# Performance work log

Measured on AMD Instinct MI355X. Metric: run time of the kernel, lower is better.

Reference implementation:

```python
import jax, jax.numpy as jnp
import numpy as np

B, T, V, E, U = 4096, 80, 10000, 100, 512


def setup_inputs() -> dict:
    key = jax.random.key(0)
    ks = jax.random.split(key, 8)
    s = 0.05  # small init scale to keep tanh unsaturated
    return {
        "tokens": jax.random.randint(ks[0], (B, T), 0, V),
        "emb": jax.random.normal(ks[1], (V, E), jnp.float32),
        "W0": jax.random.normal(ks[2], (E, U), jnp.float32) * s,
        "U0": jax.random.normal(ks[3], (U, U), jnp.float32) * s,
        "b0": jnp.zeros((U,), jnp.float32),
        "W1": jax.random.normal(ks[4], (U, U), jnp.float32) * s,
        "U1": jax.random.normal(ks[5], (U, U), jnp.float32) * s,
        "b1": jnp.zeros((U,), jnp.float32),
        "Wout": jax.random.normal(ks[6], (U, 1), jnp.float32) * s,
        "bout": jnp.zeros((1,), jnp.float32),
    }


def reference(tokens, emb, W0, U0, b0, W1, U1, b1, Wout, bout):
    # Embedding lookup: [B, T, E]
    x = emb[tokens]
    batch = tokens.shape[0]
    units = W0.shape[1]
    h0 = jnp.zeros((batch, units), x.dtype)
    h1 = jnp.zeros((batch, units), x.dtype)

    def step(carry, xt):
        h0, h1 = carry
        # SimpleRNNCell (inference: dropout inactive): h' = tanh(x@W + h@U + b)
        h0 = jnp.tanh(xt @ W0 + h0 @ U0 + b0)
        h1 = jnp.tanh(h0 @ W1 + h1 @ U1 + b1)
        return (h0, h1), None

    (h0, h1), _ = jax.lax.scan(step, (h0, h1), jnp.swapaxes(x, 0, 1))  # time-major scan
    return jax.nn.sigmoid(h1 @ Wout + bout)  # [B, 1]
```

## Files before the change

### kernel.cpp

```cpp
#include <hip/hip_runtime.h>
#include <hip/hip_bf16.h>
#include <math.h>

#define Tt 80
#define Vv 10000
#define Ee 100
#define Uu 512
#define ROWS 16
#define NBLK 256
#define SLICE_B 32768
#define NSLICE 24

typedef __attribute__((ext_vector_type(4))) int i32x4;
typedef __attribute__((ext_vector_type(4))) unsigned u32x4;

__device__ __forceinline__ i32x4 as_i4(u32x4 v) {
    union { u32x4 u; i32x4 i; } p;
    p.u = v;
    return p.i;
}

__device__ __forceinline__ float tanh_fast(float x) {
    float z = fminf(fmaxf(x, -15.f), 15.f);
    float e = __expf(2.f * z);
    return (e - 1.f) / (e + 1.f);
}

__global__ __launch_bounds__(512) void k_embw0(const float* __restrict__ emb,
                                               const float* __restrict__ W0,
                                               const float* __restrict__ b0,
                                               float* __restrict__ embW0) {
    __shared__ float semb[4][Ee];
    int v0 = blockIdx.x * 4;
    int tid = threadIdx.x;
    if (tid < 4 * Ee) semb[tid / Ee][tid % Ee] = emb[(v0 + tid / Ee) * Ee + tid % Ee];
    __syncthreads();
    float b = b0[tid];
    for (int vl = 0; vl < 4; ++vl) {
        float a = 0.f;
        #pragma unroll 4
        for (int e = 0; e < Ee; ++e) a += semb[vl][e] * W0[e * Uu + tid];
        embW0[(v0 + vl) * Uu + tid] = a + b;
    }
}

__global__ __launch_bounds__(256) void k_scale(const float* __restrict__ U0,
                                               const float* __restrict__ W1,
                                               const float* __restrict__ U1,
                                               float* __restrict__ scl) {
    int w = blockIdx.x * 4 + (threadIdx.x >> 6);
    int lane = threadIdx.x & 63;
    int mat = w >> 9, col = w & 511;
    const float* src = (mat == 0) ? U0 : (mat == 1) ? W1 : U1;
    float v = 0.f;
    #pragma unroll
    for (int i = 0; i < 8; ++i) v = fmaxf(v, fabsf(src[(lane + i * 64) * Uu + col]));
    #pragma unroll
    for (int o = 32; o; o >>= 1) v = fmaxf(v, __shfl_xor(v, o));
    if (lane == 0) scl[w] = v;
}

__global__ __launch_bounds__(256) void k_pack(const float* __restrict__ U0,
                                              const float* __restrict__ W1,
                                              const float* __restrict__ U1,
                                              const float* __restrict__ scl,
                                              char* __restrict__ pW) {
    int gid = blockIdx.x * 256 + threadIdx.x;
    int S = gid >> 11;
    int ntg = (gid >> 6) & 31;
    int lane = gid & 63;
    int col = ntg * 16 + (lane & 15);
    const float* src;
    int slot;
    float a;
    if (S < 8) { src = U0; slot = S; a = scl[col]; }
    else {
        int s2 = S - 8;
        slot = s2 >> 1;
        src = (s2 & 1) ? U1 : W1;
        a = fmaxf(scl[512 + col], scl[1024 + col]);
    }
    float inv = 127.0f / a;
    int k0 = slot * 64 + (lane >> 4) * 16;
    union { char c[16]; uint4 u; } v;
    #pragma unroll
    for (int j = 0; j < 16; ++j) {
        int q = (int)rintf(src[(k0 + j) * Uu + col] * inv);
        q = q > 127 ? 127 : (q < -127 ? -127 : q);
        v.c[j] = (char)q;
    }
    *(uint4*)(pW + (size_t)gid * 16) = v.u;
}

#define VMW(N) do { asm volatile("s_waitcnt vmcnt(" #N ")" ::: "memory"); \
    __builtin_amdgcn_sched_barrier(0); } while (0)

#define LG_SYNC() do { asm volatile("s_waitcnt lgkmcnt(0)" ::: "memory"); \
    __builtin_amdgcn_sched_barrier(0); __builtin_amdgcn_s_barrier(); \
    __builtin_amdgcn_sched_barrier(0); } while (0)

#define BISSUE(S, slot) do { \
    const char* wa_ = pWb + wvoff + (size_t)(S) * SLICE_B; \
    asm volatile("global_load_dwordx4 %0, %2, off\n\t" \
                 "global_load_dwordx4 %1, %2, off offset:1024" \
                 : "=&v"(bf[slot][0]), "=&v"(bf[slot][1]) \
                 : "v"(wa_)); \
} while (0)

#define GISSUE(T) do { \
    _Pragma("unroll") \
    for (int r_ = 0; r_ < 4; ++r_) { \
        int tk_ = stok[(q * 4 + r_) * Tt + (T)]; \
        const float* ga_ = embW0 + (size_t)tk_ * Uu + wv * 32 + ln; \
        asm volatile("global_load_dword %0, %2, off\n\t" \
                     "global_load_dword %1, %2, off offset:64" \
                     : "=&v"(gx[0][r_]), "=&v"(gx[1][r_]) \
                     : "v"(ga_)); \
    } \
} while (0)

__global__ __launch_bounds__(1024, 4)
void k_rnn(const int* __restrict__ tokens,
           const float* __restrict__ embW0,
           const char* __restrict__ pWu,
           const float* __restrict__ scl,
           const float* __restrict__ b1,
           const float* __restrict__ Wout,
           const float* __restrict__ bout,
           float* __restrict__ out) {
    __shared__ __align__(16) char smem[32768 + ROWS * Tt * 4];
    char* h0c = smem;
    char* h0f = smem + 8192;
    char* h1c = smem + 16384;
    char* h1f = smem + 24576;
    int* stok = (int*)(smem + 32768);
    float* finalb = (float*)smem;

    const int tid = threadIdx.x;
    const int lane = tid & 63;
    const int wv = tid >> 6;
    const int q = lane >> 4;
    const int ln = lane & 15;
    const int bbase = blockIdx.x * ROWS;
    const int swz = (ln & 7) << 4;
    const char* pWb = pWu;
    const int wvoff = wv * 2048 + lane * 16;
    const float r127 = 1.0f / 127.0f;

    {
        uint4 z = {0u, 0u, 0u, 0u};
        #pragma unroll
        for (int i = 0; i < 2; ++i) ((uint4*)smem)[tid + i * 1024] = z;
    }
    for (int i = tid; i < ROWS * Tt; i += 1024) stok[i] = tokens[bbase * Tt + i];

    float DQ0[2], DQ1[2], b1c[2];
    #pragma unroll
    for (int n = 0; n < 2; ++n) {
        int col = wv * 32 + n * 16 + ln;
        DQ0[n] = scl[col] / 16129.0f;
        DQ1[n] = fmaxf(scl[512 + col], scl[1024 + col]) / 16129.0f;
        b1c[n] = b1[col];
    }
    float wout8[8];
    #pragma unroll
    for (int j = 0; j < 8; ++j) wout8[j] = Wout[lane * 8 + j];
    float boutv = bout[0];

    __syncthreads();

    u32x4 bf[3][2];
    float gx[2][4];

    GISSUE(0);
    BISSUE(0, 0);
    BISSUE(1, 1);
    VMW(4);

    for (int t = 0; t < Tt; ++t) {
        i32x4 accC[2], accF[2];
        #pragma unroll
        for (int n = 0; n < 2; ++n)
            #pragma unroll
            for (int r = 0; r < 4; ++r) { accC[n][r] = 0; accF[n][r] = 0; }

        #pragma unroll
        for (int p = 0; p < 8; ++p) {
            VMW(2);
            BISSUE(p + 2, (p + 2) % 3);
            int off = (ln * 512 + p * 64 + q * 16) ^ swz;
            i32x4 aC = *(const i32x4*)(h0c + off);
            i32x4 aF = *(const i32x4*)(h0f + off);
            #pragma unroll
            for (int n = 0; n < 2; ++n) {
                accC[n] = __builtin_amdgcn_mfma_i32_16x16x64_i8(aC, as_i4(bf[p % 3][n]), accC[n], 0, 0, 0);
                accF[n] = __builtin_amdgcn_mfma_i32_16x16x64_i8(aF, as_i4(bf[p % 3][n]), accF[n], 0, 0, 0);
            }
        }

        float th0[2][4];
        #pragma unroll
        for (int n = 0; n < 2; ++n)
            #pragma unroll
            for (int r = 0; r < 4; ++r)
                th0[n][r] = tanh_fast(gx[n][r] + DQ0[n] * ((float)accC[n][r] + (float)accF[n][r] * r127));

        LG_SYNC();
        #pragma unroll
        for (int n = 0; n < 2; ++n)
            #pragma unroll
            for (int r = 0; r < 4; ++r) {
                int row = q * 4 + r;
                int col = wv * 32 + n * 16 + ln;
                int off = (row * 512 + col) ^ ((row & 7) << 4);
                float t127 = th0[n][r] * 127.f;
                float hc = rintf(t127);
                h0c[off] = (char)(int)hc;
                h0f[off] = (char)(int)rintf((t127 - hc) * 127.f);
            }
        LG_SYNC();

        GISSUE(t + 1 < Tt ? t + 1 : 0);

        i32x4 a1C[2], a1F[2];
        #pragma unroll
        for (int n = 0; n < 2; ++n)
            #pragma unroll
            for (int r = 0; r < 4; ++r) { a1C[n][r] = 0; a1F[n][r] = 0; }

        #pragma unroll
        for (int p = 8; p < 24; ++p) {
            if (p < 10) { VMW(10); }
            else        { VMW(2);  }
            BISSUE((p + 2) % NSLICE, (p + 2) % 3);
            const int idx = p - 8;
            const int k2 = idx >> 1;
            const char* hc_ = (idx & 1) ? h1c : h0c;
            const char* hf_ = (idx & 1) ? h1f : h0f;
            int off = (ln * 512 + k2 * 64 + q * 16) ^ swz;
            i32x4 aC = *(const i32x4*)(hc_ + off);
            i32x4 aF = *(const i32x4*)(hf_ + off);
            #pragma unroll
            for (int n = 0; n < 2; ++n) {
                a1C[n] = __builtin_amdgcn_mfma_i32_16x16x64_i8(aC, as_i4(bf[p % 3][n]), a1C[n], 0, 0, 0);
                a1F[n] = __builtin_amdgcn_mfma_i32_16x16x64_i8(aF, as_i4(bf[p % 3][n]), a1F[n], 0, 0, 0);
            }
        }

        float th1[2][4];
        #pragma unroll
        for (int n = 0; n < 2; ++n)
            #pragma unroll
            for (int r = 0; r < 4; ++r)
                th1[n][r] = tanh_fast(b1c[n] + DQ1[n] * ((float)a1C[n][r] + (float)a1F[n][r] * r127));

        LG_SYNC();
        if (t < Tt - 1) {
            #pragma unroll
            for (int n = 0; n < 2; ++n)
                #pragma unroll
                for (int r = 0; r < 4; ++r) {
                    int row = q * 4 + r;
                    int col = wv * 32 + n * 16 + ln;
                    int off = (row * 512 + col) ^ ((row & 7) << 4);
                    float t127 = th1[n][r] * 127.f;
                    float hc = rintf(t127);
                    h1c[off] = (char)(int)hc;
                    h1f[off] = (char)(int)rintf((t127 - hc) * 127.f);
                }
        } else {
            #pragma unroll
            for (int n = 0; n < 2; ++n)
                #pragma unroll
                for (int r = 0; r < 4; ++r)
                    finalb[(q * 4 + r) * Uu + wv * 32 + n * 16 + ln] = th1[n][r];
        }
    }

    asm volatile("s_waitcnt vmcnt(0) lgkmcnt(0)" ::: "memory");
    __builtin_amdgcn_sched_barrier(0);
    __builtin_amdgcn_s_barrier();
    __builtin_amdgcn_sched_barrier(0);

    {
        float s = 0.f;
        #pragma unroll
        for (int j = 0; j < 8; ++j)
            s += finalb[wv * Uu + lane * 8 + j] * wout8[j];
        #pragma unroll
        for (int off = 32; off; off >>= 1) s += __shfl_xor(s, off);
        if (lane == 0) out[bbase + wv] = 1.f / (1.f + __expf(-(s + boutv)));
    }
}

extern "C" void kernel_launch(void* const* d_in, const int* in_sizes, int n_in,
                              void* d_out, int out_size, void* d_ws, size_t ws_size,
                              hipStream_t stream) {
    const int*   tokens = (const int*)d_in[0];
    const float* emb    = (const float*)d_in[1];
    const float* W0     = (const float*)d_in[2];
    const float* U0     = (const float*)d_in[3];
    const float* b0     = (const float*)d_in[4];
    const float* W1     = (const float*)d_in[5];
    const float* U1     = (const float*)d_in[6];
    const float* b1     = (const float*)d_in[7];
    const float* Wout   = (const float*)d_in[8];
    const float* bout   = (const float*)d_in[9];
    float* outp = (float*)d_out;

    char* ws = (char*)d_ws;
    float* embW0 = (float*)ws;
    char* pW = ws + 20480000;
    float* scl = (float*)(ws + 20480000 + 786432);

    hipLaunchKernelGGL(k_embw0, dim3(Vv / 4), dim3(512), 0, stream, emb, W0, b0, embW0);
    hipLaunchKernelGGL(k_scale, dim3(384), dim3(256), 0, stream, U0, W1, U1, scl);
    hipLaunchKernelGGL(k_pack, dim3(192), dim3(256), 0, stream, U0, W1, U1, scl, pW);
    hipLaunchKernelGGL(k_rnn, dim3(NBLK), dim3(1024), 0, stream,
                       tokens, embW0, pW, scl, b1, Wout, bout, outp);
}
```

Baseline: 886.1 us.

## Cache first three U0 weight slices in LDS instead of streaming from global

The first three of the 24 int8 weight slices (the U0 part) are copied once per block into about 96KB of shared memory. Each timestep's first three MFMA k-steps then read B operands from LDS, and the global prefetch ring now streams only slices 3-23, with the wait counts and ring indices remapped to match. This cuts per-step global and L2 weight traffic by an eighth. In exchange, shared memory per block grows to about 136KB, which forbids running more than one 1024-thread block per CU, and the Wout and bout registers are dropped in favour of direct loads at the end.

```diff
diff --git a/kernel.cpp b/kernel.cpp
--- a/kernel.cpp
+++ b/kernel.cpp
@@ -128,12 +128,13 @@
            const float* __restrict__ Wout,
            const float* __restrict__ bout,
            float* __restrict__ out) {
-    __shared__ __align__(16) char smem[32768 + ROWS * Tt * 4];
+    __shared__ __align__(16) char smem[136192];
     char* h0c = smem;
     char* h0f = smem + 8192;
     char* h1c = smem + 16384;
     char* h1f = smem + 24576;
     int* stok = (int*)(smem + 32768);
+    char* ldsW = smem + 37888;
     float* finalb = (float*)smem;
 
     const int tid = threadIdx.x;
@@ -153,6 +154,13 @@
         for (int i = 0; i < 2; ++i) ((uint4*)smem)[tid + i * 1024] = z;
     }
     for (int i = tid; i < ROWS * Tt; i += 1024) stok[i] = tokens[bbase * Tt + i];
+    __syncthreads();
+
+    #pragma unroll
+    for (int k = 0; k < 6; ++k) {
+        uint4 v = *(const uint4*)(pWb + ((size_t)(k * 1024 + tid)) * 16);
+        *(uint4*)(ldsW + (k * 1024 + tid) * 16) = v;
+    }
 
     float DQ0[2], DQ1[2], b1c[2];
     #pragma unroll
@@ -162,20 +170,17 @@
         DQ1[n] = fmaxf(scl[512 + col], scl[1024 + col]) / 16129.0f;
         b1c[n] = b1[col];
     }
-    float wout8[8];
-    #pragma unroll
-    for (int j = 0; j < 8; ++j) wout8[j] = Wout[lane * 8 + j];
-    float boutv = bout[0];
-
-    __syncthreads();
 
     u32x4 bf[3][2];
     float gx[2][4];
 
     GISSUE(0);
-    BISSUE(0, 0);
-    BISSUE(1, 1);
-    VMW(4);
+    asm volatile("s_waitcnt vmcnt(0)" ::: "memory");
+    __builtin_amdgcn_sched_barrier(0);
+    __syncthreads();
+
+    BISSUE(3, 0);
+    BISSUE(4, 1);
 
     for (int t = 0; t < Tt; ++t) {
         i32x4 accC[2], accF[2];
@@ -186,16 +191,24 @@
 
         #pragma unroll
         for (int p = 0; p < 8; ++p) {
-            VMW(2);
-            BISSUE(p + 2, (p + 2) % 3);
+            i32x4 bb0, bb1;
+            if (p < 3) {
+                const char* ls = ldsW + p * SLICE_B + wvoff;
+                bb0 = *(const i32x4*)ls;
+                bb1 = *(const i32x4*)(ls + 1024);
+            } else {
+                VMW(2);
+                BISSUE(p + 2, (p - 1) % 3);
+                bb0 = as_i4(bf[p % 3][0]);
+                bb1 = as_i4(bf[p % 3][1]);
+            }
             int off = (ln * 512 + p * 64 + q * 16) ^ swz;
             i32x4 aC = *(const i32x4*)(h0c + off);
             i32x4 aF = *(const i32x4*)(h0f + off);
-            #pragma unroll
-            for (int n = 0; n < 2; ++n) {
-                accC[n] = __builtin_amdgcn_mfma_i32_16x16x64_i8(aC, as_i4(bf[p % 3][n]), accC[n], 0, 0, 0);
-                accF[n] = __builtin_amdgcn_mfma_i32_16x16x64_i8(aF, as_i4(bf[p % 3][n]), accF[n], 0, 0, 0);
-            }
+            accC[0] = __builtin_amdgcn_mfma_i32_16x16x64_i8(aC, bb0, accC[0], 0, 0, 0);
+            accC[1] = __builtin_amdgcn_mfma_i32_16x16x64_i8(aC, bb1, accC[1], 0, 0, 0);
+            accF[0] = __builtin_amdgcn_mfma_i32_16x16x64_i8(aF, bb0, accF[0], 0, 0, 0);
+            accF[1] = __builtin_amdgcn_mfma_i32_16x16x64_i8(aF, bb1, accF[1], 0, 0, 0);
         }
 
         float th0[2][4];
@@ -230,9 +243,12 @@
 
         #pragma unroll
         for (int p = 8; p < 24; ++p) {
-            if (p < 10) { VMW(10); }
-            else        { VMW(2);  }
-            BISSUE((p + 2) % NSLICE, (p + 2) % 3);
+            if      (p == 8 || p == 9) { VMW(10); }
+            else if (p == 10)          { VMW(4);  }
+            else                       { VMW(2);  }
+            if      (p <= 21) BISSUE(p + 2, (p - 1) % 3);
+            else if (p == 22) BISSUE(3, 0);
+            else              BISSUE(4, 1);
             const int idx = p - 8;
             const int k2 = idx >> 1;
             const char* hc_ = (idx & 1) ? h1c : h0c;
@@ -240,11 +256,12 @@
             int off = (ln * 512 + k2 * 64 + q * 16) ^ swz;
             i32x4 aC = *(const i32x4*)(hc_ + off);
             i32x4 aF = *(const i32x4*)(hf_ + off);
-            #pragma unroll
-            for (int n = 0; n < 2; ++n) {
-                a1C[n] = __builtin_amdgcn_mfma_i32_16x16x64_i8(aC, as_i4(bf[p % 3][n]), a1C[n], 0, 0, 0);
-                a1F[n] = __builtin_amdgcn_mfma_i32_16x16x64_i8(aF, as_i4(bf[p % 3][n]), a1F[n], 0, 0, 0);
-            }
+            i32x4 bb0 = as_i4(bf[p % 3][0]);
+            i32x4 bb1 = as_i4(bf[p % 3][1]);
+            a1C[0] = __builtin_amdgcn_mfma_i32_16x16x64_i8(aC, bb0, a1C[0], 0, 0, 0);
+            a1C[1] = __builtin_amdgcn_mfma_i32_16x16x64_i8(aC, bb1, a1C[1], 0, 0, 0);
+            a1F[0] = __builtin_amdgcn_mfma_i32_16x16x64_i8(aF, bb0, a1F[0], 0, 0, 0);
+            a1F[1] = __builtin_amdgcn_mfma_i32_16x16x64_i8(aF, bb1, a1F[1], 0, 0, 0);
         }
 
         float th1[2][4];
@@ -286,10 +303,10 @@
         float s = 0.f;
         #pragma unroll
         for (int j = 0; j < 8; ++j)
-            s += finalb[wv * Uu + lane * 8 + j] * wout8[j];
+            s += finalb[wv * Uu + lane * 8 + j] * Wout[lane * 8 + j];
         #pragma unroll
         for (int off = 32; off; off >>= 1) s += __shfl_xor(s, off);
-        if (lane == 0) out[bbase + wv] = 1.f / (1.f + __expf(-(s + boutv)));
+        if (lane == 0) out[bbase + wv] = 1.f / (1.f + __expf(-(s + bout[0])));
     }
 }
 
```

Result: no change. 884.3 us, median of 2 (-0.2%).
